# Performance work log

Hardware: AMD Instinct MI355X
Metric: run time of the kernel (lower is better)

## Reference

```python
import jax, jax.numpy as jnp
import numpy as np

MAX_JOINTS = 143

def setup_inputs() -> dict:
    key = jax.random.key(0)
    ks = jax.random.split(key, 8)
    d_model, latent_dim, feat = 256, 512, 13
    s = lambda n: 1.0 / np.sqrt(n)
    return {
        "z": jax.random.normal(ks[0], (32, latent_dim), jnp.float32),
        "W_latent": jax.random.normal(ks[1], (latent_dim, d_model), jnp.float32) * s(latent_dim),
        "b_latent": jnp.zeros((d_model,), jnp.float32),
        "joint_emb": jax.random.normal(ks[2], (MAX_JOINTS, d_model), jnp.float32),
        "frame_emb": jax.random.normal(ks[3], (120, d_model), jnp.float32),
        "ln_gamma": jnp.ones((d_model,), jnp.float32),
        "ln_beta": jnp.zeros((d_model,), jnp.float32),
        "W1": jax.random.normal(ks[4], (d_model, d_model), jnp.float32) * s(d_model),
        "b1": jnp.zeros((d_model,), jnp.float32),
        "W2": jax.random.normal(ks[5], (d_model, feat), jnp.float32) * s(d_model),
        "b2": jnp.zeros((feat,), jnp.float32),
        "max_frames": 120,
    }

def reference(z, W_latent, b_latent, joint_emb, frame_emb, ln_gamma, ln_beta, W1, b1, W2, b2, max_frames):
    # base: [B, d]
    base = z @ W_latent + b_latent
    fe = frame_emb[:max_frames]  # [F, d]
    # three-way broadcast sum -> [B, J, F, d]
    hidden = base[:, None, None, :] + joint_emb[None, :, None, :] + fe[None, None, :, :]
    # LayerNorm over last dim (eps=1e-5, torch default)
    mu = jnp.mean(hidden, axis=-1, keepdims=True)
    var = jnp.mean(jnp.square(hidden - mu), axis=-1, keepdims=True)
    h = (hidden - mu) * jax.lax.rsqrt(var + 1e-5) * ln_gamma + ln_beta
    # MLP: Linear -> exact GELU -> Linear
    h = jax.nn.gelu(h @ W1 + b1, approximate=False)
    out = h @ W2 + b2  # [B, J, F, feat]
    return jnp.transpose(out, (0, 1, 3, 2))  # [B, J, feat, F]
```

## Files before the change

kernel.cpp:

```cpp
#include <hip/hip_runtime.h>
#include <hip/hip_bf16.h>

typedef __bf16 bf16x8 __attribute__((ext_vector_type(8)));
typedef float  f32x4  __attribute__((ext_vector_type(4)));
typedef float  f32x2  __attribute__((ext_vector_type(2)));

#define B_  32
#define J_  143
#define F_  120
#define D_  256
#define L_  512
#define C_  13
#define M_  4576
#define MP_ 4736
#define FE0 4576
#define NK  512
#define NN  384
#define QB  6
#define GRIDC 763

static __device__ __forceinline__ unsigned short bits(__bf16 h) {
  return __builtin_bit_cast(unsigned short, h);
}

__device__ __forceinline__ f32x2 gelu2(f32x2 u) {
  f32x2 x2 = u * u;
  f32x2 t  = u * (x2 * -0.1029432f + -2.3022082f);
  f32x2 e;
  e.x = __builtin_amdgcn_exp2f(t.x);
  e.y = __builtin_amdgcn_exp2f(t.y);
  f32x2 d = e + 1.0f;
  f32x2 r;
  r.x = __builtin_amdgcn_rcpf(d.x);
  r.y = __builtin_amdgcn_rcpf(d.y);
  return u * r;
}

__global__ __launch_bounds__(256) void prepAll_kernel(
    const float* __restrict__ z, const float* __restrict__ Wl,
    const float* __restrict__ bl, const float* __restrict__ W1,
    const float* __restrict__ gamma, const float* __restrict__ beta,
    const float* __restrict__ b1, const float* __restrict__ fe,
    const float* __restrict__ W2,
    float* __restrict__ base, unsigned short* __restrict__ BT,
    float* __restrict__ bW1, float* __restrict__ Sfe, float* __restrict__ Sfe2,
    unsigned short* __restrict__ W2T, float* __restrict__ zerov) {
  const int t = threadIdx.x, bid = blockIdx.x;
  const int lane = t & 63, wv = t >> 6;
  __shared__ float zs[L_];
  __shared__ float ra[4], rb[4];
  if (bid < 32) {
    zs[t]       = z[bid * L_ + t];
    zs[t + 256] = z[bid * L_ + t + 256];
    __syncthreads();
    float acc = 0.f;
    #pragma unroll 32
    for (int k = 0; k < L_; ++k) acc = __builtin_fmaf(zs[k], Wl[k * D_ + t], acc);
    base[bid * D_ + t] = acc + bl[t];
    return;
  }
  const int n = bid - 32;
  if (n < 256) {
    const float w1v = W1[t * D_ + n];
    float a = gamma[t] * w1v;
    float b = beta[t] * w1v;
    const float wg = a;
    #pragma unroll
    for (int m = 1; m < 64; m <<= 1) { a += __shfl_xor(a, m); b += __shfl_xor(b, m); }
    if (lane == 0) { ra[wv] = a; rb[wv] = b; }
    __syncthreads();
    const float cs = ra[0] + ra[1] + ra[2] + ra[3];
    if (t == 0) bW1[n] = rb[0] + rb[1] + rb[2] + rb[3] + b1[n];
    const float m = __builtin_fmaf(cs, -1.f / 256.f, wg);
    const __bf16 hi = (__bf16)m;
    const __bf16 lo = (__bf16)(m - (float)hi);
    BT[n * NK + t]       = bits(hi);
    BT[n * NK + 256 + t] = bits(lo);
  } else if (n < 376) {
    const int f = n - 256;
    const float v = fe[f * D_ + t];
    float a = v, b = v * v;
    #pragma unroll
    for (int m = 1; m < 64; m <<= 1) { a += __shfl_xor(a, m); b += __shfl_xor(b, m); }
    if (lane == 0) { ra[wv] = a; rb[wv] = b; }
    __syncthreads();
    if (t == 0) {
      Sfe[f]  = ra[0] + ra[1] + ra[2] + ra[3];
      Sfe2[f] = rb[0] + rb[1] + rb[2] + rb[3];
    }
    const __bf16 hi = (__bf16)v;
    const __bf16 lo = (__bf16)(v - (float)hi);
    BT[n * NK + t]       = bits(hi);
    BT[n * NK + 256 + t] = bits(lo);
  } else if (n < 384) {
    BT[n * NK + t] = 0; BT[n * NK + 256 + t] = 0;
  } else if (n < 400) {
    const int c = n - 384;
    const float v = (c < C_) ? W2[t * C_ + c] : 0.f;
    W2T[c * D_ + t] = bits((__bf16)v);
  } else {
    zerov[t] = 0.f;
  }
}

__global__ __launch_bounds__(256, 4) void gemmB_kernel(
    const float* __restrict__ base, const float* __restrict__ joint,
    const float* __restrict__ fe, const float* __restrict__ zerov,
    const unsigned short* __restrict__ BT,
    float* __restrict__ PX, float* __restrict__ Sc, float* __restrict__ Sc2) {
  const int tid = threadIdx.x, lane = tid & 63, wave = tid >> 6;
  const int lrow = lane & 15, lgrp = lane >> 4;
  const int rb_ = blockIdx.x / 6, cb_ = blockIdx.x % 6;
  const int rowbase = rb_ * 32 + (wave & 1) * 16;
  const int colbase = cb_ * 64 + (wave >> 1) * 32;
  const int r = rowbase + lrow;

  const float *p1, *p2;
  if (r < M_) {
    const int b = r / J_, j = r - b * J_;
    p1 = base + b * D_; p2 = joint + j * D_;
  } else if (r < FE0 + F_) {
    p1 = fe + (r - FE0) * D_; p2 = zerov;
  } else {
    p1 = zerov; p2 = zerov;
  }

  const unsigned short* Bp = BT + (size_t)(colbase + lrow) * NK + lgrp * 8;
  f32x4 acc[2] = {};
  float ssum = 0.f, ssq = 0.f;
  const bool doSum = (cb_ == 0) && ((wave >> 1) == 0);
  #pragma unroll
  for (int s8 = 0; s8 < 8; ++s8) {
    const int k0 = s8 * 32 + lgrp * 8;
    const float4 ca = *(const float4*)(p1 + k0);
    const float4 cb4 = *(const float4*)(p1 + k0 + 4);
    const float4 da = *(const float4*)(p2 + k0);
    const float4 db = *(const float4*)(p2 + k0 + 4);
    const float c[8] = {ca.x + da.x, ca.y + da.y, ca.z + da.z, ca.w + da.w,
                        cb4.x + db.x, cb4.y + db.y, cb4.z + db.z, cb4.w + db.w};
    bf16x8 ahi, alo;
    #pragma unroll
    for (int e = 0; e < 8; ++e) {
      const __bf16 h = (__bf16)c[e];
      ahi[e] = h;
      alo[e] = (__bf16)(c[e] - (float)h);
    }
    if (doSum) {
      #pragma unroll
      for (int e = 0; e < 8; ++e) { ssum += c[e]; ssq = __builtin_fmaf(c[e], c[e], ssq); }
    }
    bf16x8 bhi[2], blo[2];
    #pragma unroll
    for (int nf = 0; nf < 2; ++nf) {
      bhi[nf] = *(const bf16x8*)(Bp + (size_t)nf * 16 * NK + s8 * 32);
      blo[nf] = *(const bf16x8*)(Bp + (size_t)nf * 16 * NK + 256 + s8 * 32);
    }
    #pragma unroll
    for (int nf = 0; nf < 2; ++nf) {
      acc[nf] = __builtin_amdgcn_mfma_f32_16x16x32_bf16(ahi, bhi[nf], acc[nf], 0, 0, 0);
      acc[nf] = __builtin_amdgcn_mfma_f32_16x16x32_bf16(alo, bhi[nf], acc[nf], 0, 0, 0);
      acc[nf] = __builtin_amdgcn_mfma_f32_16x16x32_bf16(ahi, blo[nf], acc[nf], 0, 0, 0);
    }
  }

  if (doSum) {
    ssum += __shfl_xor(ssum, 16); ssum += __shfl_xor(ssum, 32);
    ssq  += __shfl_xor(ssq, 16);  ssq  += __shfl_xor(ssq, 32);
    if (lgrp == 0) { Sc[r] = ssum; Sc2[r] = ssq; }
  }

  #pragma unroll
  for (int nf = 0; nf < 2; ++nf)
    #pragma unroll
    for (int r4 = 0; r4 < 4; ++r4)
      PX[(size_t)(rowbase + lgrp * 4 + r4) * NN + colbase + nf * 16 + lrow] = acc[nf][r4];
}

__global__ __launch_bounds__(256, 3) void mainC_kernel(
    const float* __restrict__ PX, const float* __restrict__ bW1,
    const float* __restrict__ Sc, const float* __restrict__ Sc2,
    const float* __restrict__ Sfe, const float* __restrict__ Sfe2,
    const unsigned short* __restrict__ W2T, const float* __restrict__ b2,
    float* __restrict__ out) {
  __shared__ float pc[QB][256], bw[256], rstdl[QB][128];
  __shared__ __align__(16) unsigned short w2l[4096];
  const int tid = threadIdx.x, lane = tid & 63, wv = tid >> 6;
  const int lrow = lane & 15, lgrp = lane >> 4;
  const int bj0 = blockIdx.x * QB;

  #pragma unroll
  for (int q = 0; q < QB; ++q) pc[q][tid] = PX[(size_t)(bj0 + q) * NN + tid];
  bw[tid] = bW1[tid];
  {
    const int rr = tid >> 4;
    const int b0 = tid * 32;
    const int sb = b0 ^ ((rr & 7) << 4);
    *(uint4*)((char*)w2l + sb)        = *(const uint4*)((const char*)W2T + b0);
    *(uint4*)((char*)w2l + (sb ^ 16)) = *(const uint4*)((const char*)W2T + b0 + 16);
  }
  #pragma unroll
  for (int qq = 0; qq < 3; ++qq) {
    const int idx = tid + qq * 256;
    const int q = idx >> 7;
    const int f = idx & 127;
    const int fc = f < F_ ? f : F_ - 1;
    const float X = PX[(size_t)(bj0 + q) * NN + 256 + fc];
    const float mu = (Sc[bj0 + q] + Sfe[fc]) * (1.f / 256.f);
    const float ms = __builtin_fmaf(2.f, X, Sc2[bj0 + q] + Sfe2[fc]) * (1.f / 256.f);
    rstdl[q][f] = rsqrtf(ms - mu * mu + 1e-5f);
  }
  __syncthreads();

  const int r0 = wv * 32 + lrow, r1 = r0 + 16;
  const int f0 = r0 < F_ ? r0 : F_ - 1;
  const int f1 = r1 < F_ ? r1 : F_ - 1;
  float rs0[QB], rs1[QB];
  #pragma unroll
  for (int q = 0; q < QB; ++q) { rs0[q] = rstdl[q][r0]; rs1[q] = rstdl[q][r1]; }
  const float* __restrict__ q0p = PX + (size_t)(FE0 + f0) * NN + lgrp * 8;
  const float* __restrict__ q1p = PX + (size_t)(FE0 + f1) * NN + lgrp * 8;

  float4 qa0 = *(const float4*)(q0p), qa1 = *(const float4*)(q0p + 4);
  float4 qb0 = *(const float4*)(q1p), qb1 = *(const float4*)(q1p + 4);

  f32x4 acc[QB][2] = {};
  #pragma unroll
  for (int s = 0; s < 8; ++s) {
    const int n0 = s * 32 + lgrp * 8;
    float4 na0, na1, nb0, nb1;
    if (s < 7) {
      na0 = *(const float4*)(q0p + (s + 1) * 32);
      na1 = *(const float4*)(q0p + (s + 1) * 32 + 4);
      nb0 = *(const float4*)(q1p + (s + 1) * 32);
      nb1 = *(const float4*)(q1p + (s + 1) * 32 + 4);
    }
    const bf16x8 w2f = *(const bf16x8*)((const char*)w2l +
        ((lrow * 512 + n0 * 2) ^ ((lrow & 7) << 4)));
    const float q0v[8] = {qa0.x, qa0.y, qa0.z, qa0.w, qa1.x, qa1.y, qa1.z, qa1.w};
    const float q1v[8] = {qb0.x, qb0.y, qb0.z, qb0.w, qb1.x, qb1.y, qb1.z, qb1.w};
    #pragma unroll
    for (int q = 0; q < QB; ++q) {
      bf16x8 af0, af1;
      #pragma unroll
      for (int ep = 0; ep < 4; ++ep) {
        const int e0 = 2 * ep;
        f32x2 Q0, Q1, BV;
        Q0.x = q0v[e0]; Q0.y = q0v[e0 + 1];
        Q1.x = q1v[e0]; Q1.y = q1v[e0 + 1];
        BV = *(const f32x2*)(&bw[n0 + e0]);
        const f32x2 P = *(const f32x2*)(&pc[q][n0 + e0]);
        f32x2 RS0; RS0.x = rs0[q]; RS0.y = rs0[q];
        f32x2 RS1; RS1.x = rs1[q]; RS1.y = rs1[q];
        const f32x2 U0 = __builtin_elementwise_fma(RS0, P + Q0, BV);
        const f32x2 U1 = __builtin_elementwise_fma(RS1, P + Q1, BV);
        const f32x2 G0 = gelu2(U0);
        const f32x2 G1 = gelu2(U1);
        af0[e0] = (__bf16)G0.x; af0[e0 + 1] = (__bf16)G0.y;
        af1[e0] = (__bf16)G1.x; af1[e0 + 1] = (__bf16)G1.y;
      }
      acc[q][0] = __builtin_amdgcn_mfma_f32_16x16x32_bf16(af0, w2f, acc[q][0], 0, 0, 0);
      acc[q][1] = __builtin_amdgcn_mfma_f32_16x16x32_bf16(af1, w2f, acc[q][1], 0, 0, 0);
    }
    qa0 = na0; qa1 = na1; qb0 = nb0; qb1 = nb1;
  }

  if (lrow < C_) {
    const float bias = b2[lrow];
    #pragma unroll
    for (int q = 0; q < QB; ++q) {
      if (bj0 + q < M_) {
        #pragma unroll
        for (int mf = 0; mf < 2; ++mf) {
          const int f = wv * 32 + mf * 16 + lgrp * 4;
          if (f < F_) {
            float4 v;
            v.x = acc[q][mf][0] + bias;
            v.y = acc[q][mf][1] + bias;
            v.z = acc[q][mf][2] + bias;
            v.w = acc[q][mf][3] + bias;
            *(float4*)(out + (size_t)(bj0 + q) * (C_ * F_) + lrow * F_ + f) = v;
          }
        }
      }
    }
  }
}

extern "C" void kernel_launch(void* const* d_in, const int* in_sizes, int n_in,
                              void* d_out, int out_size, void* d_ws, size_t ws_size,
                              hipStream_t stream) {
  const float* z     = (const float*)d_in[0];
  const float* Wl    = (const float*)d_in[1];
  const float* bl    = (const float*)d_in[2];
  const float* joint = (const float*)d_in[3];
  const float* fe    = (const float*)d_in[4];
  const float* gamma = (const float*)d_in[5];
  const float* beta  = (const float*)d_in[6];
  const float* W1    = (const float*)d_in[7];
  const float* b1    = (const float*)d_in[8];
  const float* W2    = (const float*)d_in[9];
  const float* b2    = (const float*)d_in[10];
  float* out = (float*)d_out;

  char* ws = (char*)d_ws;
  float*          base  = (float*)(ws + 0);
  unsigned short* W2T   = (unsigned short*)(ws + 32768);
  float*          bW1   = (float*)(ws + 40960);
  float*          Sfe   = (float*)(ws + 41984);
  float*          Sfe2  = (float*)(ws + 42496);
  float*          Sc    = (float*)(ws + 43008);
  float*          Sc2   = (float*)(ws + 61952);
  float*          zerov = (float*)(ws + 80896);
  unsigned short* BT    = (unsigned short*)(ws + 81920);
  float*          PX    = (float*)(ws + 8388608);

  prepAll_kernel<<<433, 256, 0, stream>>>(z, Wl, bl, W1, gamma, beta, b1, fe, W2,
                                          base, BT, bW1, Sfe, Sfe2, W2T, zerov);
  gemmB_kernel<<<888, 256, 0, stream>>>(base, joint, fe, zerov, BT, PX, Sc, Sc2);
  mainC_kernel<<<GRIDC, 256, 0, stream>>>(PX, bW1, Sc, Sc2, Sfe, Sfe2, W2T, b2, out);
}
```

Baseline: 85.24 us.

## Fuse projection GEMM into main kernel and precompute frame-embedding W1 projection

Removes the separate gemmB kernel and its PX workspace round trip: each block of the main kernel now builds the base+joint rows in shared memory, computes their row sums and the split-bf16 MFMA projection itself, and keeps the result in LDS. The frame-embedding projection through gamma-scaled W1 is computed once in fp32 in the prep kernel (P2f). The main kernel grows to 512 threads with 9 rows per block, with one 16-frame tile per wave. This saves a launch and global traffic, but adds redundant per-block reads of the BT matrix and more LDS per block, which may reduce occupancy.

```diff
diff --git a/kernel.cpp b/kernel.cpp
--- a/kernel.cpp
+++ b/kernel.cpp
@@ -12,12 +12,12 @@
 #define L_  512
 #define C_  13
 #define M_  4576
-#define MP_ 4736
-#define FE0 4576
 #define NK  512
-#define NN  384
-#define QB  6
-#define GRIDC 763
+#define NNB 384
+#define QB  9
+#define GRIDC 509
+#define CLS 260
+#define PXS 388
 
 static __device__ __forceinline__ unsigned short bits(__bf16 h) {
   return __builtin_bit_cast(unsigned short, h);
@@ -36,7 +36,7 @@
   return u * r;
 }
 
-__global__ __launch_bounds__(256) void prepAll_kernel(
+__global__ __launch_bounds__(256) void prep_kernel(
     const float* __restrict__ z, const float* __restrict__ Wl,
     const float* __restrict__ bl, const float* __restrict__ W1,
     const float* __restrict__ gamma, const float* __restrict__ beta,
@@ -44,11 +44,13 @@
     const float* __restrict__ W2,
     float* __restrict__ base, unsigned short* __restrict__ BT,
     float* __restrict__ bW1, float* __restrict__ Sfe, float* __restrict__ Sfe2,
-    unsigned short* __restrict__ W2T, float* __restrict__ zerov) {
+    unsigned short* __restrict__ W2T, float* __restrict__ P2f) {
   const int t = threadIdx.x, bid = blockIdx.x;
   const int lane = t & 63, wv = t >> 6;
   __shared__ float zs[L_];
   __shared__ float ra[4], rb[4];
+  __shared__ float fegl[256], gl2[256];
+
   if (bid < 32) {
     zs[t]       = z[bid * L_ + t];
     zs[t + 256] = z[bid * L_ + t + 256];
@@ -59,227 +61,235 @@
     base[bid * D_ + t] = acc + bl[t];
     return;
   }
-  const int n = bid - 32;
-  if (n < 256) {
-    const float w1v = W1[t * D_ + n];
-    float a = gamma[t] * w1v;
-    float b = beta[t] * w1v;
-    const float wg = a;
-    #pragma unroll
-    for (int m = 1; m < 64; m <<= 1) { a += __shfl_xor(a, m); b += __shfl_xor(b, m); }
-    if (lane == 0) { ra[wv] = a; rb[wv] = b; }
+  if (bid < 432) {
+    const int n = bid - 32;
+    if (n < 256) {
+      const float w1v = W1[t * D_ + n];
+      float a = gamma[t] * w1v;
+      float b = beta[t] * w1v;
+      const float wg = a;
+      #pragma unroll
+      for (int m = 1; m < 64; m <<= 1) { a += __shfl_xor(a, m); b += __shfl_xor(b, m); }
+      if (lane == 0) { ra[wv] = a; rb[wv] = b; }
+      __syncthreads();
+      const float cs = ra[0] + ra[1] + ra[2] + ra[3];
+      if (t == 0) bW1[n] = rb[0] + rb[1] + rb[2] + rb[3] + b1[n];
+      const float m = __builtin_fmaf(cs, -1.f / 256.f, wg);
+      const __bf16 hi = (__bf16)m;
+      const __bf16 lo = (__bf16)(m - (float)hi);
+      BT[n * NK + t]       = bits(hi);
+      BT[n * NK + 256 + t] = bits(lo);
+    } else if (n < 376) {
+      const int f = n - 256;
+      const float v = fe[f * D_ + t];
+      float a = v, b = v * v;
+      #pragma unroll
+      for (int m = 1; m < 64; m <<= 1) { a += __shfl_xor(a, m); b += __shfl_xor(b, m); }
+      if (lane == 0) { ra[wv] = a; rb[wv] = b; }
+      __syncthreads();
+      if (t == 0) {
+        Sfe[f]  = ra[0] + ra[1] + ra[2] + ra[3];
+        Sfe2[f] = rb[0] + rb[1] + rb[2] + rb[3];
+      }
+      const __bf16 hi = (__bf16)v;
+      const __bf16 lo = (__bf16)(v - (float)hi);
+      BT[n * NK + t]       = bits(hi);
+      BT[n * NK + 256 + t] = bits(lo);
+    } else if (n < 384) {
+      BT[n * NK + t] = 0; BT[n * NK + 256 + t] = 0;
+    } else {
+      const int c = n - 384;
+      const float v = (c < C_) ? W2[t * C_ + c] : 0.f;
+      W2T[c * D_ + t] = bits((__bf16)v);
+    }
+    return;
+  }
+  {
+    const int f = bid - 432;
+    const float fv = fe[f * D_ + t];
+    const float gv = gamma[t];
+    fegl[t] = fv * gv;
+    gl2[t]  = gv;
+    float a = fv;
+    #pragma unroll
+    for (int m = 1; m < 64; m <<= 1) a += __shfl_xor(a, m);
+    if (lane == 0) ra[wv] = a;
     __syncthreads();
-    const float cs = ra[0] + ra[1] + ra[2] + ra[3];
-    if (t == 0) bW1[n] = rb[0] + rb[1] + rb[2] + rb[3] + b1[n];
-    const float m = __builtin_fmaf(cs, -1.f / 256.f, wg);
-    const __bf16 hi = (__bf16)m;
-    const __bf16 lo = (__bf16)(m - (float)hi);
-    BT[n * NK + t]       = bits(hi);
-    BT[n * NK + 256 + t] = bits(lo);
-  } else if (n < 376) {
-    const int f = n - 256;
-    const float v = fe[f * D_ + t];
-    float a = v, b = v * v;
-    #pragma unroll
-    for (int m = 1; m < 64; m <<= 1) { a += __shfl_xor(a, m); b += __shfl_xor(b, m); }
-    if (lane == 0) { ra[wv] = a; rb[wv] = b; }
-    __syncthreads();
-    if (t == 0) {
-      Sfe[f]  = ra[0] + ra[1] + ra[2] + ra[3];
-      Sfe2[f] = rb[0] + rb[1] + rb[2] + rb[3];
-    }
-    const __bf16 hi = (__bf16)v;
-    const __bf16 lo = (__bf16)(v - (float)hi);
-    BT[n * NK + t]       = bits(hi);
-    BT[n * NK + 256 + t] = bits(lo);
-  } else if (n < 384) {
-    BT[n * NK + t] = 0; BT[n * NK + 256 + t] = 0;
-  } else if (n < 400) {
-    const int c = n - 384;
-    const float v = (c < C_) ? W2[t * C_ + c] : 0.f;
-    W2T[c * D_ + t] = bits((__bf16)v);
-  } else {
-    zerov[t] = 0.f;
-  }
-}
-
-__global__ __launch_bounds__(256, 4) void gemmB_kernel(
+    const float sfe = ra[0] + ra[1] + ra[2] + ra[3];
+    float acc1 = 0.f, acc2 = 0.f;
+    #pragma unroll 8
+    for (int k = 0; k < 256; ++k) {
+      const float w = W1[k * D_ + t];
+      acc1 = __builtin_fmaf(fegl[k], w, acc1);
+      acc2 = __builtin_fmaf(gl2[k],  w, acc2);
+    }
+    P2f[f * D_ + t] = __builtin_fmaf(-sfe * (1.f / 256.f), acc2, acc1);
+  }
+}
+
+__global__ __launch_bounds__(512, 4) void megaC_kernel(
     const float* __restrict__ base, const float* __restrict__ joint,
-    const float* __restrict__ fe, const float* __restrict__ zerov,
-    const unsigned short* __restrict__ BT,
-    float* __restrict__ PX, float* __restrict__ Sc, float* __restrict__ Sc2) {
-  const int tid = threadIdx.x, lane = tid & 63, wave = tid >> 6;
-  const int lrow = lane & 15, lgrp = lane >> 4;
-  const int rb_ = blockIdx.x / 6, cb_ = blockIdx.x % 6;
-  const int rowbase = rb_ * 32 + (wave & 1) * 16;
-  const int colbase = cb_ * 64 + (wave >> 1) * 32;
-  const int r = rowbase + lrow;
-
-  const float *p1, *p2;
-  if (r < M_) {
-    const int b = r / J_, j = r - b * J_;
-    p1 = base + b * D_; p2 = joint + j * D_;
-  } else if (r < FE0 + F_) {
-    p1 = fe + (r - FE0) * D_; p2 = zerov;
-  } else {
-    p1 = zerov; p2 = zerov;
-  }
-
-  const unsigned short* Bp = BT + (size_t)(colbase + lrow) * NK + lgrp * 8;
-  f32x4 acc[2] = {};
-  float ssum = 0.f, ssq = 0.f;
-  const bool doSum = (cb_ == 0) && ((wave >> 1) == 0);
-  #pragma unroll
-  for (int s8 = 0; s8 < 8; ++s8) {
-    const int k0 = s8 * 32 + lgrp * 8;
-    const float4 ca = *(const float4*)(p1 + k0);
-    const float4 cb4 = *(const float4*)(p1 + k0 + 4);
-    const float4 da = *(const float4*)(p2 + k0);
-    const float4 db = *(const float4*)(p2 + k0 + 4);
-    const float c[8] = {ca.x + da.x, ca.y + da.y, ca.z + da.z, ca.w + da.w,
-                        cb4.x + db.x, cb4.y + db.y, cb4.z + db.z, cb4.w + db.w};
-    bf16x8 ahi, alo;
-    #pragma unroll
-    for (int e = 0; e < 8; ++e) {
-      const __bf16 h = (__bf16)c[e];
-      ahi[e] = h;
-      alo[e] = (__bf16)(c[e] - (float)h);
-    }
-    if (doSum) {
-      #pragma unroll
-      for (int e = 0; e < 8; ++e) { ssum += c[e]; ssq = __builtin_fmaf(c[e], c[e], ssq); }
-    }
-    bf16x8 bhi[2], blo[2];
-    #pragma unroll
-    for (int nf = 0; nf < 2; ++nf) {
-      bhi[nf] = *(const bf16x8*)(Bp + (size_t)nf * 16 * NK + s8 * 32);
-      blo[nf] = *(const bf16x8*)(Bp + (size_t)nf * 16 * NK + 256 + s8 * 32);
-    }
-    #pragma unroll
-    for (int nf = 0; nf < 2; ++nf) {
-      acc[nf] = __builtin_amdgcn_mfma_f32_16x16x32_bf16(ahi, bhi[nf], acc[nf], 0, 0, 0);
-      acc[nf] = __builtin_amdgcn_mfma_f32_16x16x32_bf16(alo, bhi[nf], acc[nf], 0, 0, 0);
-      acc[nf] = __builtin_amdgcn_mfma_f32_16x16x32_bf16(ahi, blo[nf], acc[nf], 0, 0, 0);
-    }
-  }
-
-  if (doSum) {
-    ssum += __shfl_xor(ssum, 16); ssum += __shfl_xor(ssum, 32);
-    ssq  += __shfl_xor(ssq, 16);  ssq  += __shfl_xor(ssq, 32);
-    if (lgrp == 0) { Sc[r] = ssum; Sc2[r] = ssq; }
-  }
-
-  #pragma unroll
-  for (int nf = 0; nf < 2; ++nf)
-    #pragma unroll
-    for (int r4 = 0; r4 < 4; ++r4)
-      PX[(size_t)(rowbase + lgrp * 4 + r4) * NN + colbase + nf * 16 + lrow] = acc[nf][r4];
-}
-
-__global__ __launch_bounds__(256, 3) void mainC_kernel(
-    const float* __restrict__ PX, const float* __restrict__ bW1,
-    const float* __restrict__ Sc, const float* __restrict__ Sc2,
+    const unsigned short* __restrict__ BT, const float* __restrict__ P2f,
+    const float* __restrict__ bW1,
     const float* __restrict__ Sfe, const float* __restrict__ Sfe2,
     const unsigned short* __restrict__ W2T, const float* __restrict__ b2,
     float* __restrict__ out) {
-  __shared__ float pc[QB][256], bw[256], rstdl[QB][128];
+  __shared__ float cl[16 * CLS];
+  __shared__ float px[16 * PXS];
+  __shared__ float bw[256];
+  __shared__ float rstdl[QB][128];
+  __shared__ float Scl[QB], Sc2l[QB];
   __shared__ __align__(16) unsigned short w2l[4096];
-  const int tid = threadIdx.x, lane = tid & 63, wv = tid >> 6;
+
+  const int tid  = threadIdx.x;
+  const int lane = tid & 63, wv = tid >> 6;
   const int lrow = lane & 15, lgrp = lane >> 4;
-  const int bj0 = blockIdx.x * QB;
+  const int bj0  = blockIdx.x * QB;
 
   #pragma unroll
-  for (int q = 0; q < QB; ++q) pc[q][tid] = PX[(size_t)(bj0 + q) * NN + tid];
-  bw[tid] = bW1[tid];
-  {
+  for (int i = 0; i < 8; ++i) {
+    const int idx = tid + i * 512;
+    const int row = idx >> 8, col = idx & 255;
+    float v = 0.f;
+    if (row < QB) {
+      const int bj = min(bj0 + row, M_ - 1);
+      const int b = bj / J_, j = bj - b * J_;
+      v = base[b * D_ + col] + joint[j * D_ + col];
+    }
+    cl[row * CLS + col] = v;
+  }
+  if (tid < 256) {
+    bw[tid] = bW1[tid];
     const int rr = tid >> 4;
     const int b0 = tid * 32;
     const int sb = b0 ^ ((rr & 7) << 4);
     *(uint4*)((char*)w2l + sb)        = *(const uint4*)((const char*)W2T + b0);
     *(uint4*)((char*)w2l + (sb ^ 16)) = *(const uint4*)((const char*)W2T + b0 + 16);
   }
+  __syncthreads();
+
+  for (int r = wv; r < QB; r += 8) {
+    const float4 v4 = *(const float4*)(cl + r * CLS + lane * 4);
+    float s = v4.x + v4.y + v4.z + v4.w;
+    float q = __builtin_fmaf(v4.x, v4.x,
+              __builtin_fmaf(v4.y, v4.y,
+              __builtin_fmaf(v4.z, v4.z, v4.w * v4.w)));
+    #pragma unroll
+    for (int m = 1; m < 64; m <<= 1) { s += __shfl_xor(s, m); q += __shfl_xor(q, m); }
+    if (lane == 0) { Scl[r] = s; Sc2l[r] = q; }
+  }
+
+  {
+    const int colbase = wv * 48;
+    f32x4 acc[3] = {};
+    #pragma unroll
+    for (int s8 = 0; s8 < 8; ++s8) {
+      const int k0 = s8 * 32 + lgrp * 8;
+      const float4 c0 = *(const float4*)(cl + lrow * CLS + k0);
+      const float4 c1 = *(const float4*)(cl + lrow * CLS + k0 + 4);
+      const float cc[8] = {c0.x, c0.y, c0.z, c0.w, c1.x, c1.y, c1.z, c1.w};
+      bf16x8 ahi, alo;
+      #pragma unroll
+      for (int e = 0; e < 8; ++e) {
+        const __bf16 h = (__bf16)cc[e];
+        ahi[e] = h;
+        alo[e] = (__bf16)(cc[e] - (float)h);
+      }
+      bf16x8 bhi[3], blo[3];
+      #pragma unroll
+      for (int cf = 0; cf < 3; ++cf) {
+        const unsigned short* bp =
+            BT + (size_t)(colbase + cf * 16 + lrow) * NK + lgrp * 8;
+        bhi[cf] = *(const bf16x8*)(bp + s8 * 32);
+        blo[cf] = *(const bf16x8*)(bp + 256 + s8 * 32);
+      }
+      #pragma unroll
+      for (int cf = 0; cf < 3; ++cf)
+        acc[cf] = __builtin_amdgcn_mfma_f32_16x16x32_bf16(ahi, bhi[cf], acc[cf], 0, 0, 0);
+      #pragma unroll
+      for (int cf = 0; cf < 3; ++cf)
+        acc[cf] = __builtin_amdgcn_mfma_f32_16x16x32_bf16(alo, bhi[cf], acc[cf], 0, 0, 0);
+      #pragma unroll
+      for (int cf = 0; cf < 3; ++cf)
+        acc[cf] = __builtin_amdgcn_mfma_f32_16x16x32_bf16(ahi, blo[cf], acc[cf], 0, 0, 0);
+    }
+    #pragma unroll
+    for (int cf = 0; cf < 3; ++cf)
+      #pragma unroll
+      for (int r4 = 0; r4 < 4; ++r4)
+        px[(lgrp * 4 + r4) * PXS + colbase + cf * 16 + lrow] = acc[cf][r4];
+  }
+  __syncthreads();
+
   #pragma unroll
-  for (int qq = 0; qq < 3; ++qq) {
-    const int idx = tid + qq * 256;
-    const int q = idx >> 7;
-    const int f = idx & 127;
-    const int fc = f < F_ ? f : F_ - 1;
-    const float X = PX[(size_t)(bj0 + q) * NN + 256 + fc];
-    const float mu = (Sc[bj0 + q] + Sfe[fc]) * (1.f / 256.f);
-    const float ms = __builtin_fmaf(2.f, X, Sc2[bj0 + q] + Sfe2[fc]) * (1.f / 256.f);
-    rstdl[q][f] = rsqrtf(ms - mu * mu + 1e-5f);
+  for (int i = 0; i < 3; ++i) {
+    const int idx = tid + i * 512;
+    if (idx < QB * 128) {
+      const int q = idx >> 7;
+      const int fr = idx & 127;
+      const int fc = fr < F_ ? fr : F_ - 1;
+      const float X = px[q * PXS + 256 + fc];
+      const float mu = (Scl[q] + Sfe[fc]) * (1.f / 256.f);
+      const float ms = __builtin_fmaf(2.f, X, Sc2l[q] + Sfe2[fc]) * (1.f / 256.f);
+      rstdl[q][fr] = rsqrtf(ms - mu * mu + 1e-5f);
+    }
   }
   __syncthreads();
 
-  const int r0 = wv * 32 + lrow, r1 = r0 + 16;
+  const int r0 = wv * 16 + lrow;
   const int f0 = r0 < F_ ? r0 : F_ - 1;
-  const int f1 = r1 < F_ ? r1 : F_ - 1;
-  float rs0[QB], rs1[QB];
+  float rs[QB];
   #pragma unroll
-  for (int q = 0; q < QB; ++q) { rs0[q] = rstdl[q][r0]; rs1[q] = rstdl[q][r1]; }
-  const float* __restrict__ q0p = PX + (size_t)(FE0 + f0) * NN + lgrp * 8;
-  const float* __restrict__ q1p = PX + (size_t)(FE0 + f1) * NN + lgrp * 8;
+  for (int q = 0; q < QB; ++q) rs[q] = rstdl[q][r0];
+  const float* __restrict__ q0p = P2f + f0 * D_ + lgrp * 8;
 
   float4 qa0 = *(const float4*)(q0p), qa1 = *(const float4*)(q0p + 4);
-  float4 qb0 = *(const float4*)(q1p), qb1 = *(const float4*)(q1p + 4);
-
-  f32x4 acc[QB][2] = {};
+
+  f32x4 acc2[QB] = {};
   #pragma unroll
   for (int s = 0; s < 8; ++s) {
     const int n0 = s * 32 + lgrp * 8;
-    float4 na0, na1, nb0, nb1;
+    float4 na0, na1;
     if (s < 7) {
       na0 = *(const float4*)(q0p + (s + 1) * 32);
       na1 = *(const float4*)(q0p + (s + 1) * 32 + 4);
-      nb0 = *(const float4*)(q1p + (s + 1) * 32);
-      nb1 = *(const float4*)(q1p + (s + 1) * 32 + 4);
     }
     const bf16x8 w2f = *(const bf16x8*)((const char*)w2l +
         ((lrow * 512 + n0 * 2) ^ ((lrow & 7) << 4)));
     const float q0v[8] = {qa0.x, qa0.y, qa0.z, qa0.w, qa1.x, qa1.y, qa1.z, qa1.w};
-    const float q1v[8] = {qb0.x, qb0.y, qb0.z, qb0.w, qb1.x, qb1.y, qb1.z, qb1.w};
     #pragma unroll
     for (int q = 0; q < QB; ++q) {
-      bf16x8 af0, af1;
+      bf16x8 af;
+      f32x2 RS; RS.x = rs[q]; RS.y = rs[q];
       #pragma unroll
       for (int ep = 0; ep < 4; ++ep) {
         const int e0 = 2 * ep;
-        f32x2 Q0, Q1, BV;
+        f32x2 Q0, BV, P;
         Q0.x = q0v[e0]; Q0.y = q0v[e0 + 1];
-        Q1.x = q1v[e0]; Q1.y = q1v[e0 + 1];
         BV = *(const f32x2*)(&bw[n0 + e0]);
-        const f32x2 P = *(const f32x2*)(&pc[q][n0 + e0]);
-        f32x2 RS0; RS0.x = rs0[q]; RS0.y = rs0[q];
-        f32x2 RS1; RS1.x = rs1[q]; RS1.y = rs1[q];
-        const f32x2 U0 = __builtin_elementwise_fma(RS0, P + Q0, BV);
-        const f32x2 U1 = __builtin_elementwise_fma(RS1, P + Q1, BV);
-        const f32x2 G0 = gelu2(U0);
-        const f32x2 G1 = gelu2(U1);
-        af0[e0] = (__bf16)G0.x; af0[e0 + 1] = (__bf16)G0.y;
-        af1[e0] = (__bf16)G1.x; af1[e0 + 1] = (__bf16)G1.y;
-      }
-      acc[q][0] = __builtin_amdgcn_mfma_f32_16x16x32_bf16(af0, w2f, acc[q][0], 0, 0, 0);
-      acc[q][1] = __builtin_amdgcn_mfma_f32_16x16x32_bf16(af1, w2f, acc[q][1], 0, 0, 0);
-    }
-    qa0 = na0; qa1 = na1; qb0 = nb0; qb1 = nb1;
+        P  = *(const f32x2*)(&px[q * PXS + n0 + e0]);
+        const f32x2 U = __builtin_elementwise_fma(RS, P + Q0, BV);
+        const f32x2 G = gelu2(U);
+        af[e0] = (__bf16)G.x; af[e0 + 1] = (__bf16)G.y;
+      }
+      acc2[q] = __builtin_amdgcn_mfma_f32_16x16x32_bf16(af, w2f, acc2[q], 0, 0, 0);
+    }
+    qa0 = na0; qa1 = na1;
   }
 
   if (lrow < C_) {
     const float bias = b2[lrow];
-    #pragma unroll
-    for (int q = 0; q < QB; ++q) {
-      if (bj0 + q < M_) {
-        #pragma unroll
-        for (int mf = 0; mf < 2; ++mf) {
-          const int f = wv * 32 + mf * 16 + lgrp * 4;
-          if (f < F_) {
-            float4 v;
-            v.x = acc[q][mf][0] + bias;
-            v.y = acc[q][mf][1] + bias;
-            v.z = acc[q][mf][2] + bias;
-            v.w = acc[q][mf][3] + bias;
-            *(float4*)(out + (size_t)(bj0 + q) * (C_ * F_) + lrow * F_ + f) = v;
-          }
+    const int f = wv * 16 + lgrp * 4;
+    if (f < F_) {
+      #pragma unroll
+      for (int q = 0; q < QB; ++q) {
+        if (bj0 + q < M_) {
+          float4 v;
+          v.x = acc2[q][0] + bias;
+          v.y = acc2[q][1] + bias;
+          v.z = acc2[q][2] + bias;
+          v.w = acc2[q][3] + bias;
+          *(float4*)(out + (size_t)(bj0 + q) * (C_ * F_) + lrow * F_ + f) = v;
         }
       }
     }
@@ -308,14 +318,11 @@
   float*          bW1   = (float*)(ws + 40960);
   float*          Sfe   = (float*)(ws + 41984);
   float*          Sfe2  = (float*)(ws + 42496);
-  float*          Sc    = (float*)(ws + 43008);
-  float*          Sc2   = (float*)(ws + 61952);
-  float*          zerov = (float*)(ws + 80896);
-  unsigned short* BT    = (unsigned short*)(ws + 81920);
-  float*          PX    = (float*)(ws + 8388608);
-
-  prepAll_kernel<<<433, 256, 0, stream>>>(z, Wl, bl, W1, gamma, beta, b1, fe, W2,
-                                          base, BT, bW1, Sfe, Sfe2, W2T, zerov);
-  gemmB_kernel<<<888, 256, 0, stream>>>(base, joint, fe, zerov, BT, PX, Sc, Sc2);
-  mainC_kernel<<<GRIDC, 256, 0, stream>>>(PX, bW1, Sc, Sc2, Sfe, Sfe2, W2T, b2, out);
-}
+  float*          P2f   = (float*)(ws + 65536);
+  unsigned short* BT    = (unsigned short*)(ws + 262144);
+
+  prep_kernel<<<552, 256, 0, stream>>>(z, Wl, bl, W1, gamma, beta, b1, fe, W2,
+                                       base, BT, bW1, Sfe, Sfe2, W2T, P2f);
+  megaC_kernel<<<GRIDC, 512, 0, stream>>>(base, joint, BT, P2f, bW1,
+                                          Sfe, Sfe2, W2T, b2, out);
+}
```

New measurement: 76.07 us. 10.8% less time.
